# Performance work log

Measured on AMD Instinct MI355X. Metric: run time of the kernel, lower is better.

## Reference

```python
import jax, jax.numpy as jnp
import numpy as np

N_NODES = 50000
N_EDGES = 800000
D_FEAT = 128
D_EDGE = 64
N_HEADS = 4
OUT_DIM = 32
HID = N_HEADS * OUT_DIM  # 128


def segment_softmax(logits, seg, num_segments):
    # jraph.segment_softmax: subtract per-segment max, exp, normalize by per-segment sum
    seg_max = jax.ops.segment_max(logits, seg, num_segments=num_segments)
    e = jnp.exp(logits - seg_max[seg])
    denom = jax.ops.segment_sum(e, seg, num_segments=num_segments)
    return e / denom[seg]


def setup_inputs() -> dict:
    key = jax.random.key(0)
    ks = jax.random.split(key, 12)
    s = 1.0 / np.sqrt(D_FEAT)
    se = 1.0 / np.sqrt(D_EDGE)
    return {
        "nodes": jax.random.normal(ks[0], (N_NODES, D_FEAT), jnp.float32),
        "edges": jax.random.normal(ks[1], (N_EDGES, D_EDGE), jnp.float32),
        "senders": jax.random.randint(ks[2], (N_EDGES,), 0, N_NODES, jnp.int32),
        "receivers": jax.random.randint(ks[3], (N_EDGES,), 0, N_NODES, jnp.int32),
        "Wq": jax.random.normal(ks[4], (D_FEAT, HID), jnp.float32) * s,
        "bq": jnp.zeros((HID,), jnp.float32),
        "Wk": jax.random.normal(ks[5], (D_FEAT, HID), jnp.float32) * s,
        "bk": jnp.zeros((HID,), jnp.float32),
        "Wv": jax.random.normal(ks[6], (D_FEAT, HID), jnp.float32) * s,
        "bv": jnp.zeros((HID,), jnp.float32),
        "We": jax.random.normal(ks[7], (D_EDGE, HID), jnp.float32) * se,
        "Wu": jax.random.normal(ks[8], (D_FEAT, OUT_DIM), jnp.float32) * s,
        "bu": jnp.zeros((OUT_DIM,), jnp.float32),
    }


def reference(nodes, edges, senders, receivers, Wq, bq, Wk, bk, Wv, bv, We, Wu, bu):
    n_nodes = nodes.shape[0]
    send_feats = nodes[senders]    # [E, D]
    recv_feats = nodes[receivers]  # [E, D]

    q = (recv_feats @ Wq + bq).reshape(-1, N_HEADS, OUT_DIM)
    k = (send_feats @ Wk + bk).reshape(-1, N_HEADS, OUT_DIM)
    v = (send_feats @ Wv + bv).reshape(-1, N_HEADS, OUT_DIM)
    e = (edges @ We).reshape(-1, N_HEADS, OUT_DIM)

    attn = (q * k).sum(-1) / jnp.sqrt(jnp.asarray(OUT_DIM, q.dtype))  # [E, H]
    attn = segment_softmax(attn, receivers, n_nodes)                  # [E, H]

    msgs = (attn[:, :, None] * (v + e)).mean(axis=1)                  # [E, OUT_DIM]
    aggr = jax.ops.segment_sum(msgs, receivers, num_segments=n_nodes) # [N, OUT_DIM]

    feats = nodes @ Wu + bu
    return jax.nn.relu(feats + aggr)
```

## Files before the change

kernel.cpp:

```cpp
#include <hip/hip_runtime.h>
#include <math.h>

#define N_NODES 50000
#define N_EDGES 800000
#define D_FEAT 128
#define D_EDGE 64
#define HID 128
#define OUT_DIM 32

typedef unsigned short u16;
typedef short bf16x8 __attribute__((ext_vector_type(8)));
typedef float f32x4 __attribute__((ext_vector_type(4)));

__device__ __forceinline__ u16 f2bf(float x) {
    unsigned u = __float_as_uint(x);
    unsigned r = (u >> 16) & 1u;
    return (u16)((u + 0x7FFFu + r) >> 16);
}
__device__ __forceinline__ float bf2f(u16 s) { return __uint_as_float(((unsigned)s) << 16); }
__device__ __forceinline__ float bflo(unsigned u) { return __uint_as_float(u << 16); }
__device__ __forceinline__ float bfhi(unsigned u) { return __uint_as_float(u & 0xFFFF0000u); }

__global__ void zero_i32(int* __restrict__ p, int n) {
    int i = blockIdx.x * 256 + threadIdx.x;
    if (i < n) p[i] = 0;
}

__global__ void prep_weights(const float* __restrict__ Wq, const float* __restrict__ Wk,
                             const float* __restrict__ Wv, const float* __restrict__ We,
                             u16* __restrict__ WT_all, u16* __restrict__ WeTg) {
    int id = blockIdx.x * 256 + threadIdx.x;
    if (id < 49152) {
        int m = id >> 14, rem = id & 16383;
        int c = rem >> 7, k = rem & 127;
        const float* W = (m == 0) ? Wq : (m == 1) ? Wk : Wv;
        WT_all[id] = f2bf(W[k * HID + c]);
    } else {
        int j = id - 49152;
        int c = j >> 6, k = j & 63;
        WeTg[j] = f2bf(We[k * HID + c]);
    }
}

__global__ __launch_bounds__(256) void node_qkv_v2(
    const float* __restrict__ nodes, const u16* __restrict__ WT_all,
    const float* __restrict__ bq, const float* __restrict__ bk, const float* __restrict__ bv,
    u16* __restrict__ Q, u16* __restrict__ Kk, u16* __restrict__ Vp)
{
    __shared__ __align__(16) u16 Alds[4][32 * 136];

    const int tid = threadIdx.x;
    const int wave = tid >> 6, lane = tid & 63;
    const int quad = lane >> 4, l15 = lane & 15;
    const int rowbase = blockIdx.x * 128 + wave * 32;

    u16* As = &Alds[wave][0];
    #pragma unroll
    for (int it = 0; it < 16; ++it) {
        int idx = lane + it * 64;
        int row = idx >> 5, k4 = (idx & 31) * 4;
        float4 v = make_float4(0.f, 0.f, 0.f, 0.f);
        if (rowbase + row < N_NODES)
            v = *(const float4*)&nodes[(size_t)(rowbase + row) * D_FEAT + k4];
        ushort4 b;
        b.x = f2bf(v.x); b.y = f2bf(v.y); b.z = f2bf(v.z); b.w = f2bf(v.w);
        *(ushort4*)&As[row * 136 + k4] = b;
    }

    bf16x8 afr[2][4];
    #pragma unroll
    for (int rt = 0; rt < 2; ++rt)
        #pragma unroll
        for (int ks = 0; ks < 4; ++ks)
            afr[rt][ks] = *(const bf16x8*)&As[(rt * 16 + l15) * 136 + ks * 32 + quad * 8];

    #pragma unroll
    for (int m = 0; m < 3; ++m) {
        const u16* WT = WT_all + (size_t)m * 16384;
        const float* bvec = (m == 0) ? bq : (m == 1) ? bk : bv;
        u16* C = (m == 0) ? Q : (m == 1) ? Kk : Vp;

        f32x4 acc[2][8];
        #pragma unroll
        for (int rt = 0; rt < 2; ++rt)
            #pragma unroll
            for (int ct = 0; ct < 8; ++ct)
                acc[rt][ct] = (f32x4){0.f, 0.f, 0.f, 0.f};

        #pragma unroll
        for (int ks = 0; ks < 4; ++ks) {
            #pragma unroll
            for (int ct = 0; ct < 8; ++ct) {
                bf16x8 b = *(const bf16x8*)&WT[(ct * 16 + l15) * 128 + ks * 32 + quad * 8];
                acc[0][ct] = __builtin_amdgcn_mfma_f32_16x16x32_bf16(afr[0][ks], b, acc[0][ct], 0, 0, 0);
                acc[1][ct] = __builtin_amdgcn_mfma_f32_16x16x32_bf16(afr[1][ks], b, acc[1][ct], 0, 0, 0);
            }
        }

        #pragma unroll
        for (int ct = 0; ct < 8; ++ct) {
            int cbase = ct * 16 + l15;
            float bias = bvec[cbase];
            int oidx = (m == 2) ? ((cbase & 31) * 4 + (cbase >> 5)) : cbase;
            #pragma unroll
            for (int rt = 0; rt < 2; ++rt)
                #pragma unroll
                for (int r = 0; r < 4; ++r) {
                    int n = rowbase + rt * 16 + quad * 4 + r;
                    if (n < N_NODES)
                        C[(size_t)n * HID + oidx] = f2bf(acc[rt][ct][r] + bias);
                }
        }
    }
}

__global__ void hist_kernel(const int* __restrict__ receivers, int* __restrict__ count) {
    int e = blockIdx.x * 256 + threadIdx.x;
    atomicAdd(&count[receivers[e]], 1);
}

__global__ __launch_bounds__(256) void scan1(const int* __restrict__ count,
                                             int* __restrict__ incl, int* __restrict__ bsum) {
    __shared__ int sh[256];
    int gid = blockIdx.x * 256 + threadIdx.x;
    int v = (gid < N_NODES) ? count[gid] : 0;
    sh[threadIdx.x] = v; __syncthreads();
    #pragma unroll
    for (int off = 1; off < 256; off <<= 1) {
        int t = (threadIdx.x >= off) ? sh[threadIdx.x - off] : 0;
        __syncthreads();
        sh[threadIdx.x] += t;
        __syncthreads();
    }
    if (gid < N_NODES) incl[gid] = sh[threadIdx.x];
    if (threadIdx.x == 255) bsum[blockIdx.x] = sh[255];
}

__global__ __launch_bounds__(256) void scan2(const int* __restrict__ bsum,
                                             int* __restrict__ boff, int nblocks) {
    __shared__ int sh[256];
    int v = (threadIdx.x < nblocks) ? bsum[threadIdx.x] : 0;
    sh[threadIdx.x] = v; __syncthreads();
    #pragma unroll
    for (int off = 1; off < 256; off <<= 1) {
        int t = (threadIdx.x >= off) ? sh[threadIdx.x - off] : 0;
        __syncthreads();
        sh[threadIdx.x] += t;
        __syncthreads();
    }
    boff[threadIdx.x] = sh[threadIdx.x] - v;
}

__global__ __launch_bounds__(256) void scan3(const int* __restrict__ incl,
                                             const int* __restrict__ count,
                                             const int* __restrict__ boff,
                                             int* __restrict__ startp, int* __restrict__ cursor) {
    int gid = blockIdx.x * 256 + threadIdx.x;
    if (gid < N_NODES) {
        int ex = incl[gid] - count[gid] + boff[blockIdx.x];
        startp[gid] = ex;
        cursor[gid] = ex;
    }
    if (gid == 0) startp[N_NODES] = N_EDGES;
}

__global__ void scatter_v2(const int* __restrict__ senders, const int* __restrict__ receivers,
                           int* __restrict__ cursor, int* __restrict__ epos,
                           int* __restrict__ ssend, int* __restrict__ srecv) {
    int e = blockIdx.x * 256 + threadIdx.x;
    int r = receivers[e];
    int s = senders[e];
    int pos = atomicAdd(&cursor[r], 1);
    epos[e] = pos;
    ssend[pos] = s;
    srecv[pos] = r;
}

__global__ __launch_bounds__(256) void edge_logits_v3(
    const u16* __restrict__ Q, const u16* __restrict__ K,
    const int* __restrict__ ssend, const int* __restrict__ srecv,
    float* __restrict__ wbuf)
{
    int id = blockIdx.x * 256 + threadIdx.x;
    int i = id >> 1, half = id & 1;
    int s = ssend[i], r = srecv[i];
    const uint4* qp = (const uint4*)&Q[(size_t)r * HID + half * 64];
    const uint4* kp = (const uint4*)&K[(size_t)s * HID + half * 64];
    float a0 = 0.f, a1 = 0.f;
    #pragma unroll
    for (int j = 0; j < 4; ++j) {
        uint4 a = qp[j], b = kp[j];
        a0 += bflo(a.x) * bflo(b.x) + bfhi(a.x) * bfhi(b.x);
        a0 += bflo(a.y) * bflo(b.y) + bfhi(a.y) * bfhi(b.y);
        a0 += bflo(a.z) * bflo(b.z) + bfhi(a.z) * bfhi(b.z);
        a0 += bflo(a.w) * bflo(b.w) + bfhi(a.w) * bfhi(b.w);
    }
    #pragma unroll
    for (int j = 4; j < 8; ++j) {
        uint4 a = qp[j], b = kp[j];
        a1 += bflo(a.x) * bflo(b.x) + bfhi(a.x) * bfhi(b.x);
        a1 += bflo(a.y) * bflo(b.y) + bfhi(a.y) * bfhi(b.y);
        a1 += bflo(a.z) * bflo(b.z) + bfhi(a.z) * bfhi(b.z);
        a1 += bflo(a.w) * bflo(b.w) + bfhi(a.w) * bfhi(b.w);
    }
    const float sc = 0.17677669529663687f;
    float2 o = make_float2(expf(a0 * sc), expf(a1 * sc));
    *(float2*)&wbuf[(size_t)i * 4 + half * 2] = o;
}

__global__ __launch_bounds__(256) void denom_inv(
    const int* __restrict__ startp, const float* __restrict__ wbuf,
    float* __restrict__ inv4)
{
    int id = blockIdx.x * 256 + threadIdx.x;
    int n = id >> 2, j = id & 3;
    if (n >= N_NODES) return;
    int s = startp[n], e = startp[n + 1];
    float4 a = make_float4(0.f, 0.f, 0.f, 0.f);
    for (int i = s + j; i < e; i += 4) {
        float4 w = *(const float4*)&wbuf[(size_t)i * 4];
        a.x += w.x; a.y += w.y; a.z += w.z; a.w += w.w;
    }
    #pragma unroll
    for (int off = 1; off < 4; off <<= 1) {
        a.x += __shfl_xor(a.x, off);
        a.y += __shfl_xor(a.y, off);
        a.z += __shfl_xor(a.z, off);
        a.w += __shfl_xor(a.w, off);
    }
    if (j == 0) {
        float4 iv;
        iv.x = 0.25f / a.x; iv.y = 0.25f / a.y; iv.z = 0.25f / a.z; iv.w = 0.25f / a.w;
        *(float4*)&inv4[(size_t)n * 4] = iv;
    }
}

__global__ __launch_bounds__(256) void edge_messages_v7(
    const float* __restrict__ edges, const u16* __restrict__ WeTg,
    const u16* __restrict__ Vp, const float* __restrict__ wbuf,
    const int* __restrict__ senders, const int* __restrict__ receivers,
    const int* __restrict__ epos, const float* __restrict__ inv4,
    u16* __restrict__ msg)
{
    __shared__ __align__(16) u16 Ae[4][32 * 72];

    const int tid = threadIdx.x;
    const int wave = tid >> 6, lane = tid & 63;
    const int quad = lane >> 4, l15 = lane & 15;
    const int e0w = blockIdx.x * 128 + wave * 32;

    int snd8[8], pos8[8];
    float w8[8][4];
    #pragma unroll
    for (int idx = 0; idx < 8; ++idx) {
        int el = e0w + (idx >> 2) * 16 + quad * 4 + (idx & 3);
        snd8[idx] = senders[el];
        pos8[idx] = epos[el];
        int r = receivers[el];
        float4 w  = *(const float4*)&wbuf[(size_t)pos8[idx] * 4];
        float4 iv = *(const float4*)&inv4[(size_t)r * 4];
        w8[idx][0] = w.x * iv.x; w8[idx][1] = w.y * iv.y;
        w8[idx][2] = w.z * iv.z; w8[idx][3] = w.w * iv.w;
    }

    u16* As = &Ae[wave][0];
    #pragma unroll
    for (int it = 0; it < 8; ++it) {
        int idx = lane + it * 64;
        int row = idx >> 4, k4 = (idx & 15) * 4;
        float4 v = *(const float4*)&edges[(size_t)(e0w + row) * D_EDGE + k4];
        ushort4 b;
        b.x = f2bf(v.x); b.y = f2bf(v.y); b.z = f2bf(v.z); b.w = f2bf(v.w);
        *(ushort4*)&As[row * 72 + k4] = b;
    }

    bf16x8 afr[2][2];
    #pragma unroll
    for (int rt = 0; rt < 2; ++rt)
        #pragma unroll
        for (int ks = 0; ks < 2; ++ks)
            afr[rt][ks] = *(const bf16x8*)&As[(rt * 16 + l15) * 72 + ks * 32 + quad * 8];

    #pragma unroll
    for (int p = 0; p < 2; ++p) {
        const int d = p * 16 + l15;
        ushort4 vp8[8];
        #pragma unroll
        for (int idx = 0; idx < 8; ++idx)
            vp8[idx] = *(const ushort4*)&Vp[(size_t)snd8[idx] * HID + d * 4];

        f32x4 acc[2][4];
        #pragma unroll
        for (int rt = 0; rt < 2; ++rt)
            #pragma unroll
            for (int c = 0; c < 4; ++c)
                acc[rt][c] = (f32x4){0.f, 0.f, 0.f, 0.f};

        #pragma unroll
        for (int ks = 0; ks < 2; ++ks) {
            #pragma unroll
            for (int c = 0; c < 4; ++c) {
                bf16x8 b = *(const bf16x8*)&WeTg[((2 * c + p) * 16 + l15) * 64 + ks * 32 + quad * 8];
                acc[0][c] = __builtin_amdgcn_mfma_f32_16x16x32_bf16(afr[0][ks], b, acc[0][c], 0, 0, 0);
                acc[1][c] = __builtin_amdgcn_mfma_f32_16x16x32_bf16(afr[1][ks], b, acc[1][c], 0, 0, 0);
            }
        }

        #pragma unroll
        for (int idx = 0; idx < 8; ++idx) {
            int rt = idx >> 2, r = idx & 3;
            float out = w8[idx][0] * (acc[rt][0][r] + bf2f(vp8[idx].x))
                      + w8[idx][1] * (acc[rt][1][r] + bf2f(vp8[idx].y))
                      + w8[idx][2] * (acc[rt][2][r] + bf2f(vp8[idx].z))
                      + w8[idx][3] * (acc[rt][3][r] + bf2f(vp8[idx].w));
            msg[(size_t)pos8[idx] * OUT_DIM + d] = f2bf(out);
        }
    }
}

__global__ __launch_bounds__(256) void aggregate3(
    const u16* __restrict__ msg, const float* __restrict__ nodes,
    const float* __restrict__ Wu, const float* __restrict__ bu,
    const int* __restrict__ startp, float* __restrict__ out)
{
    int id = blockIdx.x * 256 + threadIdx.x;
    int n = id >> 5, d = id & 31;
    float acc = bu[d];
    #pragma unroll 4
    for (int i = 0; i < D_FEAT; ++i)
        acc += nodes[(size_t)n * D_FEAT + i] * Wu[i * OUT_DIM + d];
    int s = startp[n], e = startp[n + 1];
    for (int i = s; i < e; ++i)
        acc += bf2f(msg[(size_t)i * OUT_DIM + d]);
    out[id] = fmaxf(acc, 0.f);
}

extern "C" void kernel_launch(void* const* d_in, const int* in_sizes, int n_in,
                              void* d_out, int out_size, void* d_ws, size_t ws_size,
                              hipStream_t stream) {
    const float* nodes     = (const float*)d_in[0];
    const float* edges     = (const float*)d_in[1];
    const int*   senders   = (const int*)d_in[2];
    const int*   receivers = (const int*)d_in[3];
    const float* Wq = (const float*)d_in[4];
    const float* bq = (const float*)d_in[5];
    const float* Wk = (const float*)d_in[6];
    const float* bk = (const float*)d_in[7];
    const float* Wv = (const float*)d_in[8];
    const float* bv = (const float*)d_in[9];
    const float* We = (const float*)d_in[10];
    const float* Wu = (const float*)d_in[11];
    const float* bu = (const float*)d_in[12];
    float* out = (float*)d_out;

    char* p = (char*)d_ws;
    u16* Qb    = (u16*)p; p += (size_t)N_NODES * HID * 2;
    u16* Kb    = (u16*)p; p += (size_t)N_NODES * HID * 2;
    u16* Vperm = (u16*)p; p += (size_t)N_NODES * HID * 2;
    u16* WT_all= (u16*)p; p += (size_t)3 * HID * HID * 2;
    u16* WeTg  = (u16*)p; p += (size_t)HID * D_EDGE * 2;
    float* wbuf = (float*)p; p += (size_t)N_EDGES * 4 * 4;
    u16* msg   = (u16*)p; p += (size_t)N_EDGES * OUT_DIM * 2;
    float* inv4 = (float*)p; p += (size_t)N_NODES * 4 * 4;
    int* count  = (int*)p; p += (size_t)N_NODES * 4;
    int* incl   = (int*)p; p += (size_t)N_NODES * 4;
    int* startp = (int*)p; p += (size_t)(N_NODES + 4) * 4;
    int* cursor = (int*)p; p += (size_t)N_NODES * 4;
    int* epos   = (int*)p; p += (size_t)N_EDGES * 4;
    int* ssend  = (int*)p; p += (size_t)N_EDGES * 4;
    int* srecv  = (int*)p; p += (size_t)N_EDGES * 4;
    int* bsum   = (int*)p; p += 256 * 4;
    int* boff   = (int*)p; p += 256 * 4;

    const int SCAN_BLOCKS = (N_NODES + 255) / 256;

    hipLaunchKernelGGL(zero_i32, dim3(SCAN_BLOCKS), dim3(256), 0, stream, count, N_NODES);
    hipLaunchKernelGGL(hist_kernel, dim3(N_EDGES / 256), dim3(256), 0, stream,
                       receivers, count);
    hipLaunchKernelGGL(scan1, dim3(SCAN_BLOCKS), dim3(256), 0, stream, count, incl, bsum);
    hipLaunchKernelGGL(scan2, dim3(1), dim3(256), 0, stream, bsum, boff, SCAN_BLOCKS);
    hipLaunchKernelGGL(scan3, dim3(SCAN_BLOCKS), dim3(256), 0, stream,
                       incl, count, boff, startp, cursor);
    hipLaunchKernelGGL(scatter_v2, dim3(N_EDGES / 256), dim3(256), 0, stream,
                       senders, receivers, cursor, epos, ssend, srecv);
    hipLaunchKernelGGL(prep_weights, dim3(57344 / 256), dim3(256), 0, stream,
                       Wq, Wk, Wv, We, WT_all, WeTg);
    hipLaunchKernelGGL(node_qkv_v2, dim3((N_NODES + 127) / 128), dim3(256), 0, stream,
                       nodes, WT_all, bq, bk, bv, Qb, Kb, Vperm);
    hipLaunchKernelGGL(edge_logits_v3, dim3(N_EDGES * 2 / 256), dim3(256), 0, stream,
                       Qb, Kb, ssend, srecv, wbuf);
    hipLaunchKernelGGL(denom_inv, dim3((N_NODES * 4 + 255) / 256), dim3(256), 0, stream,
                       startp, wbuf, inv4);
    hipLaunchKernelGGL(edge_messages_v7, dim3(N_EDGES / 128), dim3(256), 0, stream,
                       edges, WeTg, Vperm, wbuf, senders, receivers, epos, inv4, msg);
    hipLaunchKernelGGL(aggregate3, dim3(N_NODES * OUT_DIM / 256), dim3(256), 0, stream,
                       msg, nodes, Wu, bu, startp, out);
}
```

Before: 668.8 us.

## Iterate edge messages in receiver-sorted order and load edge rows directly into MFMA fragments

The scatter kernel now writes, for each sorted slot, the original edge index instead of a per-edge position. The message kernel walks edges in receiver-sorted order: it reads wbuf, senders and receivers contiguously and writes msg coalesced, but gathers edge feature rows through the permutation. The LDS staging of edge features is dropped, and each lane converts its own fp32 values straight into bf16 MFMA fragments. The trade is scattered 256-byte edge-row reads in place of the scattered wbuf/inv4 reads and msg writes.

```diff
diff --git a/kernel.cpp b/kernel.cpp
--- a/kernel.cpp
+++ b/kernel.cpp
@@ -164,14 +164,14 @@
     if (gid == 0) startp[N_NODES] = N_EDGES;
 }
 
-__global__ void scatter_v2(const int* __restrict__ senders, const int* __restrict__ receivers,
-                           int* __restrict__ cursor, int* __restrict__ epos,
+__global__ void scatter_v3(const int* __restrict__ senders, const int* __restrict__ receivers,
+                           int* __restrict__ cursor, int* __restrict__ sorted,
                            int* __restrict__ ssend, int* __restrict__ srecv) {
     int e = blockIdx.x * 256 + threadIdx.x;
     int r = receivers[e];
     int s = senders[e];
     int pos = atomicAdd(&cursor[r], 1);
-    epos[e] = pos;
+    sorted[pos] = e;
     ssend[pos] = s;
     srecv[pos] = r;
 }
@@ -235,51 +235,52 @@
     }
 }
 
-__global__ __launch_bounds__(256) void edge_messages_v7(
+__global__ __launch_bounds__(256) void edge_messages_v8(
     const float* __restrict__ edges, const u16* __restrict__ WeTg,
     const u16* __restrict__ Vp, const float* __restrict__ wbuf,
-    const int* __restrict__ senders, const int* __restrict__ receivers,
-    const int* __restrict__ epos, const float* __restrict__ inv4,
+    const int* __restrict__ sorted, const int* __restrict__ ssend,
+    const int* __restrict__ srecv, const float* __restrict__ inv4,
     u16* __restrict__ msg)
 {
-    __shared__ __align__(16) u16 Ae[4][32 * 72];
-
     const int tid = threadIdx.x;
     const int wave = tid >> 6, lane = tid & 63;
     const int quad = lane >> 4, l15 = lane & 15;
-    const int e0w = blockIdx.x * 128 + wave * 32;
-
-    int snd8[8], pos8[8];
+    const int base = blockIdx.x * 128 + wave * 32;
+
+    int erow0 = sorted[base + l15];
+    int erow1 = sorted[base + 16 + l15];
+
+    int slot8[8], snd8[8];
     float w8[8][4];
     #pragma unroll
     for (int idx = 0; idx < 8; ++idx) {
-        int el = e0w + (idx >> 2) * 16 + quad * 4 + (idx & 3);
-        snd8[idx] = senders[el];
-        pos8[idx] = epos[el];
-        int r = receivers[el];
-        float4 w  = *(const float4*)&wbuf[(size_t)pos8[idx] * 4];
+        int sl = base + (idx >> 2) * 16 + quad * 4 + (idx & 3);
+        slot8[idx] = sl;
+        snd8[idx] = ssend[sl];
+        int r = srecv[sl];
+        float4 w  = *(const float4*)&wbuf[(size_t)sl * 4];
         float4 iv = *(const float4*)&inv4[(size_t)r * 4];
         w8[idx][0] = w.x * iv.x; w8[idx][1] = w.y * iv.y;
         w8[idx][2] = w.z * iv.z; w8[idx][3] = w.w * iv.w;
     }
 
-    u16* As = &Ae[wave][0];
-    #pragma unroll
-    for (int it = 0; it < 8; ++it) {
-        int idx = lane + it * 64;
-        int row = idx >> 4, k4 = (idx & 15) * 4;
-        float4 v = *(const float4*)&edges[(size_t)(e0w + row) * D_EDGE + k4];
-        ushort4 b;
-        b.x = f2bf(v.x); b.y = f2bf(v.y); b.z = f2bf(v.z); b.w = f2bf(v.w);
-        *(ushort4*)&As[row * 72 + k4] = b;
-    }
-
     bf16x8 afr[2][2];
     #pragma unroll
-    for (int rt = 0; rt < 2; ++rt)
-        #pragma unroll
-        for (int ks = 0; ks < 2; ++ks)
-            afr[rt][ks] = *(const bf16x8*)&As[(rt * 16 + l15) * 72 + ks * 32 + quad * 8];
+    for (int rt = 0; rt < 2; ++rt) {
+        int er = rt ? erow1 : erow0;
+        #pragma unroll
+        for (int ks = 0; ks < 2; ++ks) {
+            const float* src = &edges[(size_t)er * D_EDGE + ks * 32 + quad * 8];
+            float4 v0 = *(const float4*)src;
+            float4 v1 = *(const float4*)(src + 4);
+            bf16x8 a;
+            a[0] = (short)f2bf(v0.x); a[1] = (short)f2bf(v0.y);
+            a[2] = (short)f2bf(v0.z); a[3] = (short)f2bf(v0.w);
+            a[4] = (short)f2bf(v1.x); a[5] = (short)f2bf(v1.y);
+            a[6] = (short)f2bf(v1.z); a[7] = (short)f2bf(v1.w);
+            afr[rt][ks] = a;
+        }
+    }
 
     #pragma unroll
     for (int p = 0; p < 2; ++p) {
@@ -313,7 +314,7 @@
                       + w8[idx][1] * (acc[rt][1][r] + bf2f(vp8[idx].y))
                       + w8[idx][2] * (acc[rt][2][r] + bf2f(vp8[idx].z))
                       + w8[idx][3] * (acc[rt][3][r] + bf2f(vp8[idx].w));
-            msg[(size_t)pos8[idx] * OUT_DIM + d] = f2bf(out);
+            msg[(size_t)slot8[idx] * OUT_DIM + d] = f2bf(out);
         }
     }
 }
@@ -366,7 +367,7 @@
     int* incl   = (int*)p; p += (size_t)N_NODES * 4;
     int* startp = (int*)p; p += (size_t)(N_NODES + 4) * 4;
     int* cursor = (int*)p; p += (size_t)N_NODES * 4;
-    int* epos   = (int*)p; p += (size_t)N_EDGES * 4;
+    int* sorted = (int*)p; p += (size_t)N_EDGES * 4;
     int* ssend  = (int*)p; p += (size_t)N_EDGES * 4;
     int* srecv  = (int*)p; p += (size_t)N_EDGES * 4;
     int* bsum   = (int*)p; p += 256 * 4;
@@ -381,8 +382,8 @@
     hipLaunchKernelGGL(scan2, dim3(1), dim3(256), 0, stream, bsum, boff, SCAN_BLOCKS);
     hipLaunchKernelGGL(scan3, dim3(SCAN_BLOCKS), dim3(256), 0, stream,
                        incl, count, boff, startp, cursor);
-    hipLaunchKernelGGL(scatter_v2, dim3(N_EDGES / 256), dim3(256), 0, stream,
-                       senders, receivers, cursor, epos, ssend, srecv);
+    hipLaunchKernelGGL(scatter_v3, dim3(N_EDGES / 256), dim3(256), 0, stream,
+                       senders, receivers, cursor, sorted, ssend, srecv);
     hipLaunchKernelGGL(prep_weights, dim3(57344 / 256), dim3(256), 0, stream,
                        Wq, Wk, Wv, We, WT_all, WeTg);
     hipLaunchKernelGGL(node_qkv_v2, dim3((N_NODES + 127) / 128), dim3(256), 0, stream,
@@ -391,8 +392,8 @@
                        Qb, Kb, ssend, srecv, wbuf);
     hipLaunchKernelGGL(denom_inv, dim3((N_NODES * 4 + 255) / 256), dim3(256), 0, stream,
                        startp, wbuf, inv4);
-    hipLaunchKernelGGL(edge_messages_v7, dim3(N_EDGES / 128), dim3(256), 0, stream,
-                       edges, WeTg, Vperm, wbuf, senders, receivers, epos, inv4, msg);
+    hipLaunchKernelGGL(edge_messages_v8, dim3(N_EDGES / 128), dim3(256), 0, stream,
+                       edges, WeTg, Vperm, wbuf, sorted, ssend, srecv, inv4, msg);
     hipLaunchKernelGGL(aggregate3, dim3(N_NODES * OUT_DIM / 256), dim3(256), 0, stream,
                        msg, nodes, Wu, bu, startp, out);
 }
```

New measurement: 674.9 us. Within noise of the previous version (+0.9%).

## Fuse node update GEMM into QKV kernel and keep messages in edge order

Applied to the files above, without the earlier changes.

The nodes@Wu projection moves out of the scalar loop in the aggregate kernel and into the QKV MFMA kernel, reusing the already-loaded bf16 node fragments and writing a per-node base output. The scatter now records a sorted-position-to-edge map instead of edge-to-position. The denominator kernel writes pre-normalized softmax weights back in original edge order, so the message kernel reads them contiguously without the per-edge receiver and inverse-denominator gathers. Aggregation now gathers messages indirectly through the sorted map, trading coalesced message reads for indirect ones, and the node projection is now computed in bf16 instead of fp32.

```diff
diff --git a/kernel.cpp b/kernel.cpp
--- a/kernel.cpp
+++ b/kernel.cpp
@@ -28,6 +28,7 @@
 
 __global__ void prep_weights(const float* __restrict__ Wq, const float* __restrict__ Wk,
                              const float* __restrict__ Wv, const float* __restrict__ We,
+                             const float* __restrict__ Wu,
                              u16* __restrict__ WT_all, u16* __restrict__ WeTg) {
     int id = blockIdx.x * 256 + threadIdx.x;
     if (id < 49152) {
@@ -35,17 +36,23 @@
         int c = rem >> 7, k = rem & 127;
         const float* W = (m == 0) ? Wq : (m == 1) ? Wk : Wv;
         WT_all[id] = f2bf(W[k * HID + c]);
-    } else {
+    } else if (id < 57344) {
         int j = id - 49152;
         int c = j >> 6, k = j & 63;
         WeTg[j] = f2bf(We[k * HID + c]);
-    }
-}
-
-__global__ __launch_bounds__(256) void node_qkv_v2(
+    } else {
+        int j = id - 57344;
+        int c = j >> 7, k = j & 127;
+        WT_all[49152 + j] = f2bf(Wu[k * OUT_DIM + c]);
+    }
+}
+
+__global__ __launch_bounds__(256) void node_qkv_v3(
     const float* __restrict__ nodes, const u16* __restrict__ WT_all,
     const float* __restrict__ bq, const float* __restrict__ bk, const float* __restrict__ bv,
-    u16* __restrict__ Q, u16* __restrict__ Kk, u16* __restrict__ Vp)
+    const float* __restrict__ bu,
+    u16* __restrict__ Q, u16* __restrict__ Kk, u16* __restrict__ Vp,
+    float* __restrict__ baseout)
 {
     __shared__ __align__(16) u16 Alds[4][32 * 136];
 
@@ -112,6 +119,38 @@
                 }
         }
     }
+
+    {
+        const u16* WuT = WT_all + 49152;
+        f32x4 accu[2][2];
+        #pragma unroll
+        for (int rt = 0; rt < 2; ++rt)
+            #pragma unroll
+            for (int ct = 0; ct < 2; ++ct)
+                accu[rt][ct] = (f32x4){0.f, 0.f, 0.f, 0.f};
+        #pragma unroll
+        for (int ks = 0; ks < 4; ++ks) {
+            #pragma unroll
+            for (int ct = 0; ct < 2; ++ct) {
+                bf16x8 b = *(const bf16x8*)&WuT[(ct * 16 + l15) * 128 + ks * 32 + quad * 8];
+                accu[0][ct] = __builtin_amdgcn_mfma_f32_16x16x32_bf16(afr[0][ks], b, accu[0][ct], 0, 0, 0);
+                accu[1][ct] = __builtin_amdgcn_mfma_f32_16x16x32_bf16(afr[1][ks], b, accu[1][ct], 0, 0, 0);
+            }
+        }
+        #pragma unroll
+        for (int ct = 0; ct < 2; ++ct) {
+            int cbase = ct * 16 + l15;
+            float bias = bu[cbase];
+            #pragma unroll
+            for (int rt = 0; rt < 2; ++rt)
+                #pragma unroll
+                for (int r = 0; r < 4; ++r) {
+                    int n = rowbase + rt * 16 + quad * 4 + r;
+                    if (n < N_NODES)
+                        baseout[(size_t)n * OUT_DIM + cbase] = accu[rt][ct][r] + bias;
+                }
+        }
+    }
 }
 
 __global__ void hist_kernel(const int* __restrict__ receivers, int* __restrict__ count) {
@@ -164,14 +203,14 @@
     if (gid == 0) startp[N_NODES] = N_EDGES;
 }
 
-__global__ void scatter_v2(const int* __restrict__ senders, const int* __restrict__ receivers,
-                           int* __restrict__ cursor, int* __restrict__ epos,
+__global__ void scatter_v3(const int* __restrict__ senders, const int* __restrict__ receivers,
+                           int* __restrict__ cursor, int* __restrict__ sorted,
                            int* __restrict__ ssend, int* __restrict__ srecv) {
     int e = blockIdx.x * 256 + threadIdx.x;
     int r = receivers[e];
     int s = senders[e];
     int pos = atomicAdd(&cursor[r], 1);
-    epos[e] = pos;
+    sorted[pos] = e;
     ssend[pos] = s;
     srecv[pos] = r;
 }
@@ -208,9 +247,9 @@
     *(float2*)&wbuf[(size_t)i * 4 + half * 2] = o;
 }
 
-__global__ __launch_bounds__(256) void denom_inv(
-    const int* __restrict__ startp, const float* __restrict__ wbuf,
-    float* __restrict__ inv4)
+__global__ __launch_bounds__(256) void denom_norm3(
+    const int* __restrict__ startp, const int* __restrict__ sorted,
+    const float* __restrict__ wbuf, float* __restrict__ wnorm)
 {
     int id = blockIdx.x * 256 + threadIdx.x;
     int n = id >> 2, j = id & 3;
@@ -228,39 +267,35 @@
         a.z += __shfl_xor(a.z, off);
         a.w += __shfl_xor(a.w, off);
     }
-    if (j == 0) {
-        float4 iv;
-        iv.x = 0.25f / a.x; iv.y = 0.25f / a.y; iv.z = 0.25f / a.z; iv.w = 0.25f / a.w;
-        *(float4*)&inv4[(size_t)n * 4] = iv;
-    }
-}
-
-__global__ __launch_bounds__(256) void edge_messages_v7(
+    float4 inv;
+    inv.x = 0.25f / a.x; inv.y = 0.25f / a.y; inv.z = 0.25f / a.z; inv.w = 0.25f / a.w;
+    for (int i = s + j; i < e; i += 4) {
+        float4 w = *(const float4*)&wbuf[(size_t)i * 4];
+        w.x *= inv.x; w.y *= inv.y; w.z *= inv.z; w.w *= inv.w;
+        *(float4*)&wnorm[(size_t)sorted[i] * 4] = w;
+    }
+}
+
+__global__ __launch_bounds__(256) void edge_messages_v9(
     const float* __restrict__ edges, const u16* __restrict__ WeTg,
-    const u16* __restrict__ Vp, const float* __restrict__ wbuf,
-    const int* __restrict__ senders, const int* __restrict__ receivers,
-    const int* __restrict__ epos, const float* __restrict__ inv4,
-    u16* __restrict__ msg)
+    const u16* __restrict__ Vp, const float* __restrict__ wnorm,
+    const int* __restrict__ senders, u16* __restrict__ msg)
 {
     __shared__ __align__(16) u16 Ae[4][32 * 72];
 
     const int tid = threadIdx.x;
     const int wave = tid >> 6, lane = tid & 63;
     const int quad = lane >> 4, l15 = lane & 15;
-    const int e0w = blockIdx.x * 128 + wave * 32;
-
-    int snd8[8], pos8[8];
+    const int base = blockIdx.x * 128 + wave * 32;
+
+    int snd8[8];
     float w8[8][4];
     #pragma unroll
     for (int idx = 0; idx < 8; ++idx) {
-        int el = e0w + (idx >> 2) * 16 + quad * 4 + (idx & 3);
+        int el = base + (idx >> 2) * 16 + quad * 4 + (idx & 3);
         snd8[idx] = senders[el];
-        pos8[idx] = epos[el];
-        int r = receivers[el];
-        float4 w  = *(const float4*)&wbuf[(size_t)pos8[idx] * 4];
-        float4 iv = *(const float4*)&inv4[(size_t)r * 4];
-        w8[idx][0] = w.x * iv.x; w8[idx][1] = w.y * iv.y;
-        w8[idx][2] = w.z * iv.z; w8[idx][3] = w.w * iv.w;
+        float4 w = *(const float4*)&wnorm[(size_t)el * 4];
+        w8[idx][0] = w.x; w8[idx][1] = w.y; w8[idx][2] = w.z; w8[idx][3] = w.w;
     }
 
     u16* As = &Ae[wave][0];
@@ -268,7 +303,7 @@
     for (int it = 0; it < 8; ++it) {
         int idx = lane + it * 64;
         int row = idx >> 4, k4 = (idx & 15) * 4;
-        float4 v = *(const float4*)&edges[(size_t)(e0w + row) * D_EDGE + k4];
+        float4 v = *(const float4*)&edges[(size_t)(base + row) * D_EDGE + k4];
         ushort4 b;
         b.x = f2bf(v.x); b.y = f2bf(v.y); b.z = f2bf(v.z); b.w = f2bf(v.w);
         *(ushort4*)&As[row * 72 + k4] = b;
@@ -309,29 +344,29 @@
         #pragma unroll
         for (int idx = 0; idx < 8; ++idx) {
             int rt = idx >> 2, r = idx & 3;
+            int el = base + rt * 16 + quad * 4 + r;
             float out = w8[idx][0] * (acc[rt][0][r] + bf2f(vp8[idx].x))
                       + w8[idx][1] * (acc[rt][1][r] + bf2f(vp8[idx].y))
                       + w8[idx][2] * (acc[rt][2][r] + bf2f(vp8[idx].z))
                       + w8[idx][3] * (acc[rt][3][r] + bf2f(vp8[idx].w));
-            msg[(size_t)pos8[idx] * OUT_DIM + d] = f2bf(out);
-        }
-    }
-}
-
-__global__ __launch_bounds__(256) void aggregate3(
-    const u16* __restrict__ msg, const float* __restrict__ nodes,
-    const float* __restrict__ Wu, const float* __restrict__ bu,
-    const int* __restrict__ startp, float* __restrict__ out)
+            msg[(size_t)el * OUT_DIM + d] = f2bf(out);
+        }
+    }
+}
+
+__global__ __launch_bounds__(256) void aggregate4(
+    const u16* __restrict__ msg, const float* __restrict__ baseout,
+    const int* __restrict__ sorted, const int* __restrict__ startp,
+    float* __restrict__ out)
 {
     int id = blockIdx.x * 256 + threadIdx.x;
     int n = id >> 5, d = id & 31;
-    float acc = bu[d];
-    #pragma unroll 4
-    for (int i = 0; i < D_FEAT; ++i)
-        acc += nodes[(size_t)n * D_FEAT + i] * Wu[i * OUT_DIM + d];
+    float acc = baseout[id];
     int s = startp[n], e = startp[n + 1];
-    for (int i = s; i < e; ++i)
-        acc += bf2f(msg[(size_t)i * OUT_DIM + d]);
+    for (int i = s; i < e; ++i) {
+        int el = sorted[i];
+        acc += bf2f(msg[(size_t)el * OUT_DIM + d]);
+    }
     out[id] = fmaxf(acc, 0.f);
 }
 
@@ -357,16 +392,17 @@
     u16* Qb    = (u16*)p; p += (size_t)N_NODES * HID * 2;
     u16* Kb    = (u16*)p; p += (size_t)N_NODES * HID * 2;
     u16* Vperm = (u16*)p; p += (size_t)N_NODES * HID * 2;
-    u16* WT_all= (u16*)p; p += (size_t)3 * HID * HID * 2;
+    u16* WT_all= (u16*)p; p += (size_t)(3 * HID * HID + OUT_DIM * HID) * 2;
     u16* WeTg  = (u16*)p; p += (size_t)HID * D_EDGE * 2;
-    float* wbuf = (float*)p; p += (size_t)N_EDGES * 4 * 4;
+    float* wbuf  = (float*)p; p += (size_t)N_EDGES * 4 * 4;
+    float* wnorm = (float*)p; p += (size_t)N_EDGES * 4 * 4;
     u16* msg   = (u16*)p; p += (size_t)N_EDGES * OUT_DIM * 2;
-    float* inv4 = (float*)p; p += (size_t)N_NODES * 4 * 4;
+    float* baseout = (float*)p; p += (size_t)N_NODES * OUT_DIM * 4;
     int* count  = (int*)p; p += (size_t)N_NODES * 4;
     int* incl   = (int*)p; p += (size_t)N_NODES * 4;
     int* startp = (int*)p; p += (size_t)(N_NODES + 4) * 4;
     int* cursor = (int*)p; p += (size_t)N_NODES * 4;
-    int* epos   = (int*)p; p += (size_t)N_EDGES * 4;
+    int* sorted = (int*)p; p += (size_t)N_EDGES * 4;
     int* ssend  = (int*)p; p += (size_t)N_EDGES * 4;
     int* srecv  = (int*)p; p += (size_t)N_EDGES * 4;
     int* bsum   = (int*)p; p += 256 * 4;
@@ -381,18 +417,18 @@
     hipLaunchKernelGGL(scan2, dim3(1), dim3(256), 0, stream, bsum, boff, SCAN_BLOCKS);
     hipLaunchKernelGGL(scan3, dim3(SCAN_BLOCKS), dim3(256), 0, stream,
                        incl, count, boff, startp, cursor);
-    hipLaunchKernelGGL(scatter_v2, dim3(N_EDGES / 256), dim3(256), 0, stream,
-                       senders, receivers, cursor, epos, ssend, srecv);
-    hipLaunchKernelGGL(prep_weights, dim3(57344 / 256), dim3(256), 0, stream,
-                       Wq, Wk, Wv, We, WT_all, WeTg);
-    hipLaunchKernelGGL(node_qkv_v2, dim3((N_NODES + 127) / 128), dim3(256), 0, stream,
-                       nodes, WT_all, bq, bk, bv, Qb, Kb, Vperm);
+    hipLaunchKernelGGL(scatter_v3, dim3(N_EDGES / 256), dim3(256), 0, stream,
+                       senders, receivers, cursor, sorted, ssend, srecv);
+    hipLaunchKernelGGL(prep_weights, dim3(61440 / 256), dim3(256), 0, stream,
+                       Wq, Wk, Wv, We, Wu, WT_all, WeTg);
+    hipLaunchKernelGGL(node_qkv_v3, dim3((N_NODES + 127) / 128), dim3(256), 0, stream,
+                       nodes, WT_all, bq, bk, bv, bu, Qb, Kb, Vperm, baseout);
     hipLaunchKernelGGL(edge_logits_v3, dim3(N_EDGES * 2 / 256), dim3(256), 0, stream,
                        Qb, Kb, ssend, srecv, wbuf);
-    hipLaunchKernelGGL(denom_inv, dim3((N_NODES * 4 + 255) / 256), dim3(256), 0, stream,
-                       startp, wbuf, inv4);
-    hipLaunchKernelGGL(edge_messages_v7, dim3(N_EDGES / 128), dim3(256), 0, stream,
-                       edges, WeTg, Vperm, wbuf, senders, receivers, epos, inv4, msg);
-    hipLaunchKernelGGL(aggregate3, dim3(N_NODES * OUT_DIM / 256), dim3(256), 0, stream,
-                       msg, nodes, Wu, bu, startp, out);
-}
+    hipLaunchKernelGGL(denom_norm3, dim3((N_NODES * 4 + 255) / 256), dim3(256), 0, stream,
+                       startp, sorted, wbuf, wnorm);
+    hipLaunchKernelGGL(edge_messages_v9, dim3(N_EDGES / 128), dim3(256), 0, stream,
+                       edges, WeTg, Vperm, wnorm, senders, msg);
+    hipLaunchKernelGGL(aggregate4, dim3(N_NODES * OUT_DIM / 256), dim3(256), 0, stream,
+                       msg, baseout, sorted, startp, out);
+}
```

After: 621.9 us. -7.0%, faster.
